# Kernel tuning notes

Hardware: AMD Instinct MI355X
Metric: run time of the kernel (lower is better)

## Reference

```python
import jax, jax.numpy as jnp
import numpy as np

B, N, C, H = 4, 2048, 256, 16
D = C // H  # head dim = 16


def setup_inputs() -> dict:
    key = jax.random.key(0)
    k1, k2, k3 = jax.random.split(key, 3)
    x = jax.random.normal(k1, (B, N, C), dtype=jnp.float32)
    w_qkv = jax.random.normal(k2, (C, 3 * C), dtype=jnp.float32) * (C ** -0.5)
    b_qkv = jnp.zeros((3 * C,), dtype=jnp.float32)
    w_proj = jax.random.normal(k3, (C, C), dtype=jnp.float32) * (C ** -0.5)
    b_proj = jnp.zeros((C,), dtype=jnp.float32)
    return {"x": x, "w_qkv": w_qkv, "b_qkv": b_qkv, "w_proj": w_proj, "b_proj": b_proj}


def reference(x, w_qkv, b_qkv, w_proj, b_proj):
    b, n, c = x.shape
    qkv = x @ w_qkv + b_qkv                       # (B, N, 3C)
    qkv = qkv.reshape(b, n, 3, H, D)
    q = jnp.transpose(qkv[:, :, 0], (0, 2, 1, 3))  # (B, H, N, D)
    k = jnp.transpose(qkv[:, :, 1], (0, 2, 1, 3))
    v = jnp.transpose(qkv[:, :, 2], (0, 2, 1, 3))
    # NOTE: the original module applies NO 1/sqrt(d) scaling.
    attn = jnp.einsum('bhqd,bhkd->bhqk', q, k)     # (B, H, N, N)
    attn = jax.nn.softmax(attn, axis=-1)
    out = jnp.einsum('bhqk,bhkd->bhqd', attn, v)   # (B, H, N, D)
    out = jnp.transpose(out, (0, 2, 1, 3)).reshape(b, n, c)
    return out @ w_proj + b_proj
```

## Files before the change

kernel.cpp:

```cpp
#include <hip/hip_runtime.h>
#include <stdint.h>

typedef __attribute__((ext_vector_type(8))) short short8;
typedef __attribute__((ext_vector_type(4))) short short4v;
typedef __attribute__((ext_vector_type(4))) float float4v;
typedef __attribute__((ext_vector_type(16))) float float16v;
typedef __attribute__((ext_vector_type(4))) uint32_t uint4v;

__device__ __forceinline__ short f2bf(float f) {
    union { float f; uint32_t u; } v; v.f = f;
    uint32_t u = v.u;
    uint32_t r = (u + 0x7fffu + ((u >> 16) & 1u)) >> 16;
    return (short)r;
}

#if __has_builtin(__builtin_amdgcn_cvt_pk_bf16_f32)
typedef __bf16 bf16x2_t __attribute__((ext_vector_type(2)));
__device__ __forceinline__ uint32_t cvt_pk2(float a, float b) {
    union { bf16x2_t v; uint32_t u; } c;
    c.v = __builtin_amdgcn_cvt_pk_bf16_f32(a, b);
    return c.u;
}
#else
__device__ __forceinline__ uint32_t cvt_pk2(float a, float b) {
    union { float f; uint32_t u; } x, y; x.f = a; y.f = b;
    return ((x.u + 0x8000u) >> 16) | ((y.u + 0x8000u) & 0xFFFF0000u);
}
#endif


__global__ __launch_bounds__(256) void cvtW_kernel(const float* __restrict__ wqkv,
                                                   const float* __restrict__ wproj,
                                                   short* __restrict__ outq,
                                                   short* __restrict__ outp,
                                                   short* __restrict__ ones) {
    int idx = blockIdx.x * 256 + threadIdx.x;
    if (idx < 196608) {
        int n = idx >> 8, k = idx & 255;
        outq[idx] = f2bf(wqkv[k * 768 + n]);
    } else if (idx < 262144) {
        int i = idx - 196608;
        int n = i >> 8, k = i & 255;
        outp[i] = f2bf(wproj[k * 256 + n]);
    } else {
        int i = idx - 262144;
        if (i < 2048) ones[i] = (short)0x3F80;
    }
}


template<int MODE>
__global__ __launch_bounds__(256) void gemm_kernel(
    const void* __restrict__ Ap, const short* __restrict__ Bt,
    const float* __restrict__ bias,
    short* __restrict__ outQ, short* __restrict__ outK, short* __restrict__ outV,
    float* __restrict__ outP)
{
    const int K = 256;
    int m0 = blockIdx.x * 64;
    int n0 = blockIdx.y * 64;
    int tid = threadIdx.x;
    int wave = tid >> 6, lane = tid & 63, quad = lane >> 4, lc = lane & 15;

    __shared__ __align__(16) short As[64 * 48];
    __shared__ __align__(16) short Bs[64 * 48];

    float4v acc[4];
    #pragma unroll
    for (int t = 0; t < 4; ++t) acc[t] = (float4v){0.f, 0.f, 0.f, 0.f};

    int srow = tid >> 2, sseg = tid & 3;

    for (int c = 0; c < K; c += 32) {
        __syncthreads();
        if (MODE == 0) {
            const float* src = (const float*)Ap + (size_t)(m0 + srow) * K + c + sseg * 8;
            float4 f0 = *(const float4*)src;
            float4 f1 = *(const float4*)(src + 4);
            uint4v u; u.x = cvt_pk2(f0.x, f0.y); u.y = cvt_pk2(f0.z, f0.w);
            u.z = cvt_pk2(f1.x, f1.y); u.w = cvt_pk2(f1.z, f1.w);
            *(uint4v*)(&As[srow * 48 + sseg * 8]) = u;
        } else {
            *(short8*)(&As[srow * 48 + sseg * 8]) =
                *(const short8*)((const short*)Ap + (size_t)(m0 + srow) * K + c + sseg * 8);
        }
        *(short8*)(&Bs[srow * 48 + sseg * 8]) =
            *(const short8*)(Bt + (size_t)(n0 + srow) * K + c + sseg * 8);
        __syncthreads();

        short8 af = *(short8*)(&As[(wave * 16 + lc) * 48 + quad * 8]);
        #pragma unroll
        for (int t = 0; t < 4; ++t) {
            short8 bf = *(short8*)(&Bs[(t * 16 + lc) * 48 + quad * 8]);
            acc[t] = __builtin_amdgcn_mfma_f32_16x16x32_bf16(af, bf, acc[t], 0, 0, 0);
        }
    }

    #pragma unroll
    for (int t = 0; t < 4; ++t) {
        int cg = n0 + t * 16 + lc;
        float bv = bias[cg];
        #pragma unroll
        for (int r = 0; r < 4; ++r) {
            int rg = m0 + wave * 16 + quad * 4 + r;
            float val = acc[t][r] + bv;
            if (MODE == 0) {
                int sq = cg >> 8, rem = cg & 255, h = rem >> 4, d = rem & 15;
                int b = rg >> 11, n = rg & 2047;
                int bh = b * 16 + h;
                if (sq == 0) {
                    val *= 1.4426950408889634f;
                    outQ[((((size_t)bh) * 2048 + n) << 4) + d] = f2bf(val);
                } else if (sq == 1) {
                    outK[((((size_t)bh) * 2048 + n) << 4) + d] = f2bf(val);
                } else {
                    int sl = (n & ~12) | ((n & 4) << 1) | ((n & 8) >> 1);
                    outV[((size_t)bh * 16 + d) * 2048 + sl] = f2bf(val);
                }
            } else {
                outP[(size_t)rg * 256 + cg] = val;
            }
        }
    }
}


__global__ __launch_bounds__(256) void attn_kernel(
    const short* __restrict__ Q, const short* __restrict__ Kp,
    const short* __restrict__ Vt, const short* __restrict__ onesrow,
    short* __restrict__ Out)
{
    const int N = 2048;
    int bh = blockIdx.y;
    int b = bh >> 4, h = bh & 15;
    int tid = threadIdx.x;
    int wave = tid >> 6, lane = tid & 63;
    int m = lane & 31, hi = lane >> 5;
    int qbase = blockIdx.x * 128 + wave * 32;

    const short* Qh = Q + (size_t)bh * N * 16;
    const short* Kh = Kp + (size_t)bh * N * 16;
    const short* vbase = (m < 16) ? (Vt + ((size_t)bh * 16 + m) * 2048) : onesrow;

    short8 qf = *(const short8*)(Qh + (size_t)(qbase + m) * 16 + hi * 8);

    float16v Oacc, zf;
    #pragma unroll
    for (int j = 0; j < 16; ++j) { Oacc[j] = 0.f; zf[j] = 0.f; }

    short8 kf1 = *(const short8*)(Kh + (size_t)m * 16 + hi * 8);
    short8 kf2 = *(const short8*)(Kh + (size_t)(32 + m) * 16 + hi * 8);

    #pragma unroll 4
    for (int c = 0; c < N; c += 64) {
        float16v S1 = __builtin_amdgcn_mfma_f32_32x32x16_bf16(kf1, qf, zf, 0, 0, 0);
        float16v S2 = __builtin_amdgcn_mfma_f32_32x32x16_bf16(kf2, qf, zf, 0, 0, 0);

        int cn = (c + 64) & (N - 1);
        kf1 = *(const short8*)(Kh + (size_t)(cn + m) * 16 + hi * 8);
        kf2 = *(const short8*)(Kh + (size_t)(cn + 32 + m) * 16 + hi * 8);

        short8 vfr[4];
        #pragma unroll
        for (int p = 0; p < 4; ++p)
            vfr[p] = *(const short8*)(vbase + c + p * 16 + hi * 8);

        union { uint4v u; short8 s; } pA, pB, pC, pD;
        pA.u = (uint4v){
            cvt_pk2(__builtin_amdgcn_exp2f(S1[0]), __builtin_amdgcn_exp2f(S1[1])),
            cvt_pk2(__builtin_amdgcn_exp2f(S1[2]), __builtin_amdgcn_exp2f(S1[3])),
            cvt_pk2(__builtin_amdgcn_exp2f(S1[4]), __builtin_amdgcn_exp2f(S1[5])),
            cvt_pk2(__builtin_amdgcn_exp2f(S1[6]), __builtin_amdgcn_exp2f(S1[7]))};
        pB.u = (uint4v){
            cvt_pk2(__builtin_amdgcn_exp2f(S1[8]),  __builtin_amdgcn_exp2f(S1[9])),
            cvt_pk2(__builtin_amdgcn_exp2f(S1[10]), __builtin_amdgcn_exp2f(S1[11])),
            cvt_pk2(__builtin_amdgcn_exp2f(S1[12]), __builtin_amdgcn_exp2f(S1[13])),
            cvt_pk2(__builtin_amdgcn_exp2f(S1[14]), __builtin_amdgcn_exp2f(S1[15]))};
        pC.u = (uint4v){
            cvt_pk2(__builtin_amdgcn_exp2f(S2[0]), __builtin_amdgcn_exp2f(S2[1])),
            cvt_pk2(__builtin_amdgcn_exp2f(S2[2]), __builtin_amdgcn_exp2f(S2[3])),
            cvt_pk2(__builtin_amdgcn_exp2f(S2[4]), __builtin_amdgcn_exp2f(S2[5])),
            cvt_pk2(__builtin_amdgcn_exp2f(S2[6]), __builtin_amdgcn_exp2f(S2[7]))};
        pD.u = (uint4v){
            cvt_pk2(__builtin_amdgcn_exp2f(S2[8]),  __builtin_amdgcn_exp2f(S2[9])),
            cvt_pk2(__builtin_amdgcn_exp2f(S2[10]), __builtin_amdgcn_exp2f(S2[11])),
            cvt_pk2(__builtin_amdgcn_exp2f(S2[12]), __builtin_amdgcn_exp2f(S2[13])),
            cvt_pk2(__builtin_amdgcn_exp2f(S2[14]), __builtin_amdgcn_exp2f(S2[15]))};

        Oacc = __builtin_amdgcn_mfma_f32_32x32x16_bf16(vfr[0], pA.s, Oacc, 0, 0, 0);
        Oacc = __builtin_amdgcn_mfma_f32_32x32x16_bf16(vfr[1], pB.s, Oacc, 0, 0, 0);
        Oacc = __builtin_amdgcn_mfma_f32_32x32x16_bf16(vfr[2], pC.s, Oacc, 0, 0, 0);
        Oacc = __builtin_amdgcn_mfma_f32_32x32x16_bf16(vfr[3], pD.s, Oacc, 0, 0, 0);
    }

    float Lq = __shfl(Oacc[8], m, 64);
    float inv = 1.0f / Lq;
    uint32_t o0 = cvt_pk2(Oacc[0] * inv, Oacc[1] * inv);
    uint32_t o1 = cvt_pk2(Oacc[2] * inv, Oacc[3] * inv);
    uint32_t o2 = cvt_pk2(Oacc[4] * inv, Oacc[5] * inv);
    uint32_t o3 = cvt_pk2(Oacc[6] * inv, Oacc[7] * inv);
    short* row = Out + ((size_t)(b * 2048 + qbase + m)) * 256 + h * 16;
    uint2 w0; w0.x = o0; w0.y = o1;
    uint2 w1; w1.x = o2; w1.y = o3;
    *(uint2*)(row + hi * 4) = w0;
    *(uint2*)(row + 8 + hi * 4) = w1;
}


extern "C" void kernel_launch(void* const* d_in, const int* in_sizes, int n_in,
                              void* d_out, int out_size, void* d_ws, size_t ws_size,
                              hipStream_t stream) {
    const float* x      = (const float*)d_in[0];
    const float* w_qkv  = (const float*)d_in[1];
    const float* b_qkv  = (const float*)d_in[2];
    const float* w_proj = (const float*)d_in[3];
    const float* b_proj = (const float*)d_in[4];
    float* out = (float*)d_out;

    short* wqkvT  = (short*)d_ws;
    short* wprojT = wqkvT + 196608;
    short* Qb     = wprojT + 65536;
    short* Kb     = Qb + 2097152;
    short* VtG    = Kb + 2097152;
    short* Ab     = VtG + 2097152;
    short* onesb  = Ab + 2097152;

    cvtW_kernel<<<1040, 256, 0, stream>>>(w_qkv, w_proj, wqkvT, wprojT, onesb);

    gemm_kernel<0><<<dim3(128, 12), 256, 0, stream>>>(x, wqkvT, b_qkv, Qb, Kb, VtG, nullptr);

    attn_kernel<<<dim3(16, 64), 256, 0, stream>>>(Qb, Kb, VtG, onesb, Ab);

    gemm_kernel<1><<<dim3(128, 4), 256, 0, stream>>>(Ab, wprojT, b_proj,
                                                     nullptr, nullptr, nullptr, out);
}
```

Baseline: 138.3 us.

## Widen QKV GEMM tile to 128 columns and split attention PV accumulator chain

The QKV projection GEMM now computes two 64-column B tiles per block, so each converted A tile (fp32 x to bf16) is loaded and converted once for 128 output columns and the grid shrinks from 12 to 6 column blocks. In the attention kernel the four dependent PV MFMAs per iteration now alternate between two accumulators that are summed at the end, which shortens the MFMA dependency chain. The costs are more registers and LDS per GEMM block, fewer GEMM blocks, and one extra set of accumulator registers in attention.

```diff
diff --git a/kernel.cpp b/kernel.cpp
--- a/kernel.cpp
+++ b/kernel.cpp
@@ -49,7 +49,7 @@
 }
 
 
-template<int MODE>
+template<int MODE, int NT>
 __global__ __launch_bounds__(256) void gemm_kernel(
     const void* __restrict__ Ap, const short* __restrict__ Bt,
     const float* __restrict__ bias,
@@ -58,16 +58,18 @@
 {
     const int K = 256;
     int m0 = blockIdx.x * 64;
-    int n0 = blockIdx.y * 64;
+    int n0 = blockIdx.y * (64 * NT);
     int tid = threadIdx.x;
     int wave = tid >> 6, lane = tid & 63, quad = lane >> 4, lc = lane & 15;
 
     __shared__ __align__(16) short As[64 * 48];
-    __shared__ __align__(16) short Bs[64 * 48];
-
-    float4v acc[4];
-    #pragma unroll
-    for (int t = 0; t < 4; ++t) acc[t] = (float4v){0.f, 0.f, 0.f, 0.f};
+    __shared__ __align__(16) short Bs[NT][64 * 48];
+
+    float4v acc[NT][4];
+    #pragma unroll
+    for (int nt = 0; nt < NT; ++nt)
+        #pragma unroll
+        for (int t = 0; t < 4; ++t) acc[nt][t] = (float4v){0.f, 0.f, 0.f, 0.f};
 
     int srow = tid >> 2, sseg = tid & 3;
 
@@ -84,26 +86,32 @@
             *(short8*)(&As[srow * 48 + sseg * 8]) =
                 *(const short8*)((const short*)Ap + (size_t)(m0 + srow) * K + c + sseg * 8);
         }
-        *(short8*)(&Bs[srow * 48 + sseg * 8]) =
-            *(const short8*)(Bt + (size_t)(n0 + srow) * K + c + sseg * 8);
+        #pragma unroll
+        for (int nt = 0; nt < NT; ++nt)
+            *(short8*)(&Bs[nt][srow * 48 + sseg * 8]) =
+                *(const short8*)(Bt + (size_t)(n0 + nt * 64 + srow) * K + c + sseg * 8);
         __syncthreads();
 
         short8 af = *(short8*)(&As[(wave * 16 + lc) * 48 + quad * 8]);
         #pragma unroll
-        for (int t = 0; t < 4; ++t) {
-            short8 bf = *(short8*)(&Bs[(t * 16 + lc) * 48 + quad * 8]);
-            acc[t] = __builtin_amdgcn_mfma_f32_16x16x32_bf16(af, bf, acc[t], 0, 0, 0);
-        }
-    }
-
+        for (int nt = 0; nt < NT; ++nt)
+            #pragma unroll
+            for (int t = 0; t < 4; ++t) {
+                short8 bf = *(short8*)(&Bs[nt][(t * 16 + lc) * 48 + quad * 8]);
+                acc[nt][t] = __builtin_amdgcn_mfma_f32_16x16x32_bf16(af, bf, acc[nt][t], 0, 0, 0);
+            }
+    }
+
+    #pragma unroll
+    for (int nt = 0; nt < NT; ++nt)
     #pragma unroll
     for (int t = 0; t < 4; ++t) {
-        int cg = n0 + t * 16 + lc;
+        int cg = n0 + nt * 64 + t * 16 + lc;
         float bv = bias[cg];
         #pragma unroll
         for (int r = 0; r < 4; ++r) {
             int rg = m0 + wave * 16 + quad * 4 + r;
-            float val = acc[t][r] + bv;
+            float val = acc[nt][t][r] + bv;
             if (MODE == 0) {
                 int sq = cg >> 8, rem = cg & 255, h = rem >> 4, d = rem & 15;
                 int b = rg >> 11, n = rg & 2047;
@@ -144,9 +152,9 @@
 
     short8 qf = *(const short8*)(Qh + (size_t)(qbase + m) * 16 + hi * 8);
 
-    float16v Oacc, zf;
-    #pragma unroll
-    for (int j = 0; j < 16; ++j) { Oacc[j] = 0.f; zf[j] = 0.f; }
+    float16v Oa, Ob, zf;
+    #pragma unroll
+    for (int j = 0; j < 16; ++j) { Oa[j] = 0.f; Ob[j] = 0.f; zf[j] = 0.f; }
 
     short8 kf1 = *(const short8*)(Kh + (size_t)m * 16 + hi * 8);
     short8 kf2 = *(const short8*)(Kh + (size_t)(32 + m) * 16 + hi * 8);
@@ -187,18 +195,21 @@
             cvt_pk2(__builtin_amdgcn_exp2f(S2[12]), __builtin_amdgcn_exp2f(S2[13])),
             cvt_pk2(__builtin_amdgcn_exp2f(S2[14]), __builtin_amdgcn_exp2f(S2[15]))};
 
-        Oacc = __builtin_amdgcn_mfma_f32_32x32x16_bf16(vfr[0], pA.s, Oacc, 0, 0, 0);
-        Oacc = __builtin_amdgcn_mfma_f32_32x32x16_bf16(vfr[1], pB.s, Oacc, 0, 0, 0);
-        Oacc = __builtin_amdgcn_mfma_f32_32x32x16_bf16(vfr[2], pC.s, Oacc, 0, 0, 0);
-        Oacc = __builtin_amdgcn_mfma_f32_32x32x16_bf16(vfr[3], pD.s, Oacc, 0, 0, 0);
-    }
-
-    float Lq = __shfl(Oacc[8], m, 64);
+        Oa = __builtin_amdgcn_mfma_f32_32x32x16_bf16(vfr[0], pA.s, Oa, 0, 0, 0);
+        Ob = __builtin_amdgcn_mfma_f32_32x32x16_bf16(vfr[1], pB.s, Ob, 0, 0, 0);
+        Oa = __builtin_amdgcn_mfma_f32_32x32x16_bf16(vfr[2], pC.s, Oa, 0, 0, 0);
+        Ob = __builtin_amdgcn_mfma_f32_32x32x16_bf16(vfr[3], pD.s, Ob, 0, 0, 0);
+    }
+
+    float O0 = Oa[0] + Ob[0], O1 = Oa[1] + Ob[1], O2 = Oa[2] + Ob[2], O3 = Oa[3] + Ob[3];
+    float O4 = Oa[4] + Ob[4], O5 = Oa[5] + Ob[5], O6 = Oa[6] + Ob[6], O7 = Oa[7] + Ob[7];
+    float L8 = Oa[8] + Ob[8];
+    float Lq = __shfl(L8, m, 64);
     float inv = 1.0f / Lq;
-    uint32_t o0 = cvt_pk2(Oacc[0] * inv, Oacc[1] * inv);
-    uint32_t o1 = cvt_pk2(Oacc[2] * inv, Oacc[3] * inv);
-    uint32_t o2 = cvt_pk2(Oacc[4] * inv, Oacc[5] * inv);
-    uint32_t o3 = cvt_pk2(Oacc[6] * inv, Oacc[7] * inv);
+    uint32_t o0 = cvt_pk2(O0 * inv, O1 * inv);
+    uint32_t o1 = cvt_pk2(O2 * inv, O3 * inv);
+    uint32_t o2 = cvt_pk2(O4 * inv, O5 * inv);
+    uint32_t o3 = cvt_pk2(O6 * inv, O7 * inv);
     short* row = Out + ((size_t)(b * 2048 + qbase + m)) * 256 + h * 16;
     uint2 w0; w0.x = o0; w0.y = o1;
     uint2 w1; w1.x = o2; w1.y = o3;
@@ -227,10 +238,10 @@
 
     cvtW_kernel<<<1040, 256, 0, stream>>>(w_qkv, w_proj, wqkvT, wprojT, onesb);
 
-    gemm_kernel<0><<<dim3(128, 12), 256, 0, stream>>>(x, wqkvT, b_qkv, Qb, Kb, VtG, nullptr);
+    gemm_kernel<0, 2><<<dim3(128, 6), 256, 0, stream>>>(x, wqkvT, b_qkv, Qb, Kb, VtG, nullptr);
 
     attn_kernel<<<dim3(16, 64), 256, 0, stream>>>(Qb, Kb, VtG, onesb, Ab);
 
-    gemm_kernel<1><<<dim3(128, 4), 256, 0, stream>>>(Ab, wprojT, b_proj,
-                                                     nullptr, nullptr, nullptr, out);
-}
+    gemm_kernel<1, 1><<<dim3(128, 4), 256, 0, stream>>>(Ab, wprojT, b_proj,
+                                                        nullptr, nullptr, nullptr, out);
+}
```

Result: slower. 146.5 us (+5.9%).
